# Performance work log

Hardware: AMD Instinct MI355X
Metric: run time of the kernel (lower is better)

Reference implementation:

```python
import jax, jax.numpy as jnp
import numpy as np

NEG_SLOPE = 0.01  # torch F.leaky_relu default


def _mlp_block(x, mask, W, b):
    # x: [B,P,V,F]; mask: [B,P,V] bool; W: [H,F]; b: [H]
    h = jax.nn.leaky_relu(jnp.einsum('bpvf,hf->bpvh', x, W) + b, NEG_SLOPE)
    m = mask[..., None]
    out = jnp.where(m, h, 0.0)                                   # zeros at masked-out slots
    neg = jnp.where(m, out, -jnp.inf)
    pool = jnp.max(neg, axis=2, keepdims=True)                   # [B,P,1,H] masked max-pool
    any_valid = jnp.any(mask, axis=2)[:, :, None, None]
    pool = jnp.where(any_valid, pool, 0.0)                       # fully-masked polylines -> 0
    rep = jnp.broadcast_to(pool, out.shape)
    return jnp.concatenate([out, rep], axis=-1)                  # [B,P,V,2H]


def setup_inputs() -> dict:
    key = jax.random.key(0)
    ks = jax.random.split(key, 8)
    B, P, V, F, H = 32, 512, 32, 16, 64
    input_var = jax.random.normal(ks[0], (B, P, V, F), dtype=jnp.float32)
    input_mask = jax.random.bernoulli(ks[1], 0.8, (B, P, V))
    s = 1.0 / np.sqrt(F)
    W1 = jax.random.uniform(ks[2], (H, F), jnp.float32, -s, s)
    b1 = jax.random.uniform(ks[3], (H,), jnp.float32, -s, s)
    s2 = 1.0 / np.sqrt(2 * H)
    W2 = jax.random.uniform(ks[4], (H, 2 * H), jnp.float32, -s2, s2)
    b2 = jax.random.uniform(ks[5], (H,), jnp.float32, -s2, s2)
    W3 = jax.random.uniform(ks[6], (H, 2 * H), jnp.float32, -s2, s2)
    b3 = jax.random.uniform(ks[7], (H,), jnp.float32, -s2, s2)
    return {"input_var": input_var, "input_mask": input_mask,
            "W1": W1, "b1": b1, "W2": W2, "b2": b2, "W3": W3, "b3": b3,
            "size1": P, "size2": V}


def reference(input_var, input_mask, W1, b1, W2, b2, W3, b3, size1, size2):
    hidden = W1.shape[0]
    x = _mlp_block(input_var, input_mask, W1, b1)
    y = _mlp_block(x, input_mask, W2, b2)
    z = _mlp_block(y, input_mask, W3, b3)
    out = z[:, :, 0, -hidden:]                                   # pooled half, same across V
    out = jnp.where(jnp.any(input_mask, axis=2)[..., None], out, 0.0)
    return out
```

## Files before the change

### kernel.cpp

```cpp
#include <hip/hip_runtime.h>
#include <math.h>

namespace {

typedef _Float16 f16x8 __attribute__((ext_vector_type(8)));
typedef _Float16 f16x2 __attribute__((ext_vector_type(2)));
typedef float    f32x16 __attribute__((ext_vector_type(16)));
typedef unsigned int uint;

__device__ __forceinline__ uint pkrtz(float a, float b) {
    return __builtin_bit_cast(uint, __builtin_amdgcn_cvt_pkrtz(a, b));
}
__device__ __forceinline__ uint pk_add(uint a, uint b) {
    uint r; asm("v_pk_add_f16 %0, %1, %2" : "=v"(r) : "v"(a), "v"(b)); return r;
}
__device__ __forceinline__ uint pk_mul(uint a, uint b) {
    uint r; asm("v_pk_mul_f16 %0, %1, %2" : "=v"(r) : "v"(a), "v"(b)); return r;
}
__device__ __forceinline__ uint pk_max(uint a, uint b) {
    uint r; asm("v_pk_max_f16 %0, %1, %2" : "=v"(r) : "v"(a), "v"(b)); return r;
}

__global__ void prep_pack(const float* __restrict__ W1, const float* __restrict__ W2,
                          const float* __restrict__ W3, const int* __restrict__ M,
                          unsigned short* __restrict__ wsW, uint* __restrict__ wsM)
{
    int t = blockIdx.x * blockDim.x + threadIdx.x;
    if (t < 34 * 64) {
        int f = t >> 6, l = t & 63, nb = l & 31, kg = l >> 5;
        const float* src; int K, ki, nt2;
        if (f < 2)       { src = W1; K = 16;  ki = 0;           nt2 = f; }
        else if (f < 18) { int g = f - 2;  src = W2; K = 128; ki = g >> 1; nt2 = g & 1; }
        else             { int g = f - 18; src = W3; K = 128; ki = g >> 1; nt2 = g & 1; }
        const float* s = src + (size_t)(32 * nt2 + nb) * K + 16 * ki + 8 * kg;
        uint4 q;
        q.x = pkrtz(s[0], s[1]); q.y = pkrtz(s[2], s[3]);
        q.z = pkrtz(s[4], s[5]); q.w = pkrtz(s[6], s[7]);
        *(uint4*)(wsW + (size_t)f * 512 + l * 8) = q;
    } else if (t < 34 * 64 + 16384) {
        int bp = t - 34 * 64;
        const int4* mp = (const int4*)(M + bp * 32);
        uint bits = 0;
        #pragma unroll
        for (int i = 0; i < 8; ++i) {
            int4 v = mp[i];
            bits |= ((v.x ? 1u : 0u) | (v.y ? 2u : 0u) |
                     (v.z ? 4u : 0u) | (v.w ? 8u : 0u)) << (4 * i);
        }
        wsM[bp] = bits;
    }
}

__global__ __launch_bounds__(256, 3) void fused_mlp_v10(
    const float* __restrict__ X, const uint* __restrict__ MPK,
    const unsigned short* __restrict__ WF,
    const float* __restrict__ B1, const float* __restrict__ B2,
    const float* __restrict__ B3, float* __restrict__ OUT)
{
    __shared__ __align__(16) unsigned char sXb[4][2][4096];
    __shared__ __align__(16) _Float16 sP[4][2][64];

    const int t = threadIdx.x, w = t >> 6, l = t & 63;
    const int hb = l >> 5, mtl = (l >> 4) & 1;
    const size_t bp0 = (size_t)blockIdx.x * 8 + w * 2;

    unsigned char* sb[2] = { &sXb[w][0][0], &sXb[w][1][0] };
    _Float16*     pl[2] = { &sP[w][0][0],  &sP[w][1][0]  };

    uint wb0 = (uint)((l & 7) * 32 + mtl * 256 + ((l >> 3) & 1) * 1024 + hb * 8);
    wb0 ^= (uint)(mtl << 5);
    const uint wb1 = (wb0 + 512u) ^ 64u;
    const uint rb = (uint)(mtl * 2048 + hb * 1024 + ((l & 15) >> 1) * 4);
    const uint sel = (l & 1) ? 0x07060302u : 0x05040100u;
    const uint SL2 = pkrtz(0.01f, 0.01f);

    bool anyv[2]; uint adm[2][4][2];
    #pragma unroll
    for (int u = 0; u < 2; ++u) {
        uint mk = MPK[bp0 + u];
        anyv[u] = (mk != 0u);
        #pragma unroll
        for (int g = 0; g < 4; ++g) {
            uint nib = (mk >> (8 * g + 4 * hb)) & 15u;
            adm[u][g][0] = (nib & 1u ? 0u : 0xFC00u) | (nib & 2u ? 0u : 0xFC000000u);
            adm[u][g][1] = (nib & 4u ? 0u : 0xFC00u) | (nib & 8u ? 0u : 0xFC000000u);
        }
    }

    f16x8 a1f[2];
    #pragma unroll
    for (int u = 0; u < 2; ++u) {
        const float4* xp = (const float4*)(X + ((bp0 + u) * 32 + (l & 31)) * 16 + 8 * hb);
        float4 x0 = xp[0], x1 = xp[1];
        uint4 q;
        q.x = pkrtz(x0.x, x0.y); q.y = pkrtz(x0.z, x0.w);
        q.z = pkrtz(x1.x, x1.y); q.w = pkrtz(x1.z, x1.w);
        a1f[u] = __builtin_bit_cast(f16x8, q);
    }

    f32x16 zc;
    #pragma unroll
    for (int i = 0; i < 16; ++i) zc[i] = 0.f;

    f32x16 acc[2][2];

    {
        const _Float16* wp = (const _Float16*)WF + l * 8;
        f16x8 wf0 = *(const f16x8*)wp;
        f16x8 wf1 = *(const f16x8*)(wp + 512);
        #pragma unroll
        for (int u = 0; u < 2; ++u) {
            acc[u][0] = __builtin_amdgcn_mfma_f32_32x32x16_f16(a1f[u], wf0, zc, 0, 0, 0);
            acc[u][1] = __builtin_amdgcn_mfma_f32_32x32x16_f16(a1f[u], wf1, zc, 0, 0, 0);
        }
    }

    auto epi = [&](int u, const float* __restrict__ Bp, bool dostore) {
        unsigned char* sbu = sb[u];
        _Float16* plu = pl[u];
        #pragma unroll
        for (int nt2 = 0; nt2 < 2; ++nt2) {
            float bsc = Bp[32 * nt2 + (l & 31)];
            uint bpk = pkrtz(bsc, bsc);
            uint base = nt2 ? wb1 : wb0;
            uint pp = 0xFC00FC00u;
            #pragma unroll
            for (int g = 0; g < 4; ++g) {
                uint d01 = pkrtz(acc[u][nt2][4 * g + 0], acc[u][nt2][4 * g + 1]);
                uint d23 = pkrtz(acc[u][nt2][4 * g + 2], acc[u][nt2][4 * g + 3]);
                d01 = pk_add(d01, bpk);  d23 = pk_add(d23, bpk);
                d01 = pk_max(d01, pk_mul(d01, SL2));
                d23 = pk_max(d23, pk_mul(d23, SL2));
                if (dostore) {
                    uint2 st; st.x = d01; st.y = d23;
                    *(uint2*)(sbu + base + (g >> 1) * 2048 + (g & 1) * 16) = st;
                }
                pp = pk_max(pp, pk_add(d01, adm[u][g][0]));
                pp = pk_max(pp, pk_add(d23, adm[u][g][1]));
            }
            f16x2 ph = __builtin_bit_cast(f16x2, pp);
            float pv = fmaxf((float)ph[0], (float)ph[1]);
            pv = fmaxf(pv, __shfl_xor(pv, 32));
            pv = anyv[u] ? pv : 0.f;
            if (dostore) {
                if (l < 32) plu[32 * nt2 + (l & 31)] = (_Float16)pv;
            } else {
                if (l < 32) OUT[(bp0 + u) * 64 + 32 * nt2 + (l & 31)] = pv;
            }
        }
    };

    auto layerK = [&](int fb) {
        #pragma unroll
        for (int ki = 0; ki < 8; ++ki) {
            const _Float16* wp = (const _Float16*)WF + (size_t)(fb + 2 * ki) * 512 + l * 8;
            f16x8 wf0 = *(const f16x8*)wp;
            f16x8 wf1 = *(const f16x8*)(wp + 512);
            #pragma unroll
            for (int u = 0; u < 2; ++u) {
                f16x8 a;
                if (ki < 4) {
                    const unsigned char* p = sb[u] + rb + 256 * ki;
                    uint F0 = *(const uint*)(p + 32 * (0 ^ ki));
                    uint F1 = *(const uint*)(p + 32 * (1 ^ ki));
                    uint F2 = *(const uint*)(p + 32 * (2 ^ ki));
                    uint F3 = *(const uint*)(p + 32 * (3 ^ ki));
                    uint F4 = *(const uint*)(p + 32 * (4 ^ ki));
                    uint F5 = *(const uint*)(p + 32 * (5 ^ ki));
                    uint F6 = *(const uint*)(p + 32 * (6 ^ ki));
                    uint F7 = *(const uint*)(p + 32 * (7 ^ ki));
                    uint4 q;
                    q.x = __builtin_amdgcn_perm(F1, F0, sel);
                    q.y = __builtin_amdgcn_perm(F3, F2, sel);
                    q.z = __builtin_amdgcn_perm(F5, F4, sel);
                    q.w = __builtin_amdgcn_perm(F7, F6, sel);
                    a = __builtin_bit_cast(f16x8, q);
                } else {
                    a = *(const f16x8*)(pl[u] + 16 * (ki - 4) + 8 * hb);
                }
                acc[u][0] = __builtin_amdgcn_mfma_f32_32x32x16_f16(
                    a, wf0, ki == 0 ? zc : acc[u][0], 0, 0, 0);
                acc[u][1] = __builtin_amdgcn_mfma_f32_32x32x16_f16(
                    a, wf1, ki == 0 ? zc : acc[u][1], 0, 0, 0);
            }
        }
    };

    epi(0, B1, true);  epi(1, B1, true);
    layerK(2);
    epi(0, B2, true);  epi(1, B2, true);
    layerK(18);
    epi(0, B3, false); epi(1, B3, false);
}
}

extern "C" void kernel_launch(void* const* d_in, const int* in_sizes, int n_in,
                              void* d_out, int out_size, void* d_ws, size_t ws_size,
                              hipStream_t stream) {
    (void)in_sizes; (void)n_in; (void)ws_size; (void)out_size;
    const float* X  = (const float*)d_in[0];
    const int*   M  = (const int*)d_in[1];
    const float* W1 = (const float*)d_in[2];
    const float* B1 = (const float*)d_in[3];
    const float* W2 = (const float*)d_in[4];
    const float* B2 = (const float*)d_in[5];
    const float* W3 = (const float*)d_in[6];
    const float* B3 = (const float*)d_in[7];
    float* OUT = (float*)d_out;

    unsigned short* WF  = (unsigned short*)d_ws;
    uint*           MPK = (uint*)((char*)d_ws + 34816);

    prep_pack<<<(34 * 64 + 16384 + 255) / 256, 256, 0, stream>>>(W1, W2, W3, M, WF, MPK);
    fused_mlp_v10<<<2048, 256, 0, stream>>>(X, MPK, WF, B1, B2, B3, OUT);
}
```

Baseline: 114.8 us.

## Preload layer weights into registers and re-swizzle LDS to avoid bank conflicts

Layer-2 weight fragments (16 uint4 per lane) now load into registers at kernel start. Layer-3 weights are refilled into those registers while layer 2 runs its MFMAs, so weight fetches no longer sit on the critical path. The LDS store and read addresses get an extra XOR swizzle to cut bank conflicts during the transpose-style reads. The launch bound drops from 3 to 2 waves per SIMD to leave room for the larger register footprint, which lowers occupancy.

```diff
diff --git a/kernel.cpp b/kernel.cpp
--- a/kernel.cpp
+++ b/kernel.cpp
@@ -51,7 +51,7 @@
     }
 }
 
-__global__ __launch_bounds__(256, 3) void fused_mlp_v10(
+__global__ __launch_bounds__(256, 2) void fused_mlp_v16(
     const float* __restrict__ X, const uint* __restrict__ MPK,
     const unsigned short* __restrict__ WF,
     const float* __restrict__ B1, const float* __restrict__ B2,
@@ -61,18 +61,27 @@
     __shared__ __align__(16) _Float16 sP[4][2][64];
 
     const int t = threadIdx.x, w = t >> 6, l = t & 63;
-    const int hb = l >> 5, mtl = (l >> 4) & 1;
+    const int hb = l >> 5, mtl = (l >> 4) & 1, l3 = (l >> 3) & 1;
     const size_t bp0 = (size_t)blockIdx.x * 8 + w * 2;
 
     unsigned char* sb[2] = { &sXb[w][0][0], &sXb[w][1][0] };
     _Float16*     pl[2] = { &sP[w][0][0],  &sP[w][1][0]  };
 
-    uint wb0 = (uint)((l & 7) * 32 + mtl * 256 + ((l >> 3) & 1) * 1024 + hb * 8);
-    wb0 ^= (uint)(mtl << 5);
+    uint wb0 = (uint)((l & 7) * 32 + mtl * 256 + l3 * 1024 + hb * 8);
+    wb0 ^= (uint)((mtl << 5) ^ (l3 << 4));
     const uint wb1 = (wb0 + 512u) ^ 64u;
-    const uint rb = (uint)(mtl * 2048 + hb * 1024 + ((l & 15) >> 1) * 4);
+    uint rbA = (uint)(mtl * 2048 + hb * 1024 + ((l & 15) >> 1) * 4);
+    rbA ^= (uint)((hb << 4) ^ (mtl << 5));
+    const uint rbB = rbA ^ 32u;
     const uint sel = (l & 1) ? 0x07060302u : 0x05040100u;
     const uint SL2 = pkrtz(0.01f, 0.01f);
+
+    const unsigned short* WFb = WF + l * 8;
+
+    uint4 wreg[16];
+    #pragma unroll
+    for (int f = 0; f < 16; ++f)
+        wreg[f] = *(const uint4*)(WFb + (size_t)(2 + f) * 512);
 
     bool anyv[2]; uint adm[2][4][2];
     #pragma unroll
@@ -105,9 +114,8 @@
     f32x16 acc[2][2];
 
     {
-        const _Float16* wp = (const _Float16*)WF + l * 8;
-        f16x8 wf0 = *(const f16x8*)wp;
-        f16x8 wf1 = *(const f16x8*)(wp + 512);
+        f16x8 wf0 = *(const f16x8*)(WFb);
+        f16x8 wf1 = *(const f16x8*)(WFb + 512);
         #pragma unroll
         for (int u = 0; u < 2; ++u) {
             acc[u][0] = __builtin_amdgcn_mfma_f32_32x32x16_f16(a1f[u], wf0, zc, 0, 0, 0);
@@ -132,8 +140,10 @@
                 d01 = pk_max(d01, pk_mul(d01, SL2));
                 d23 = pk_max(d23, pk_mul(d23, SL2));
                 if (dostore) {
+                    uint wba = (base ^ (uint)(((g & 1) << 4) ^ ((g >> 1) << 5)))
+                               + (uint)((g >> 1) * 2048);
                     uint2 st; st.x = d01; st.y = d23;
-                    *(uint2*)(sbu + base + (g >> 1) * 2048 + (g & 1) * 16) = st;
+                    *(uint2*)(sbu + wba) = st;
                 }
                 pp = pk_max(pp, pk_add(d01, adm[u][g][0]));
                 pp = pk_max(pp, pk_add(d23, adm[u][g][1]));
@@ -150,30 +160,28 @@
         }
     };
 
-    auto layerK = [&](int fb) {
+    auto layerK = [&](bool refill, int fb_next) {
         #pragma unroll
         for (int ki = 0; ki < 8; ++ki) {
-            const _Float16* wp = (const _Float16*)WF + (size_t)(fb + 2 * ki) * 512 + l * 8;
-            f16x8 wf0 = *(const f16x8*)wp;
-            f16x8 wf1 = *(const f16x8*)(wp + 512);
+            f16x8 wf0 = __builtin_bit_cast(f16x8, wreg[2 * ki]);
+            f16x8 wf1 = __builtin_bit_cast(f16x8, wreg[2 * ki + 1]);
             #pragma unroll
             for (int u = 0; u < 2; ++u) {
                 f16x8 a;
                 if (ki < 4) {
-                    const unsigned char* p = sb[u] + rb + 256 * ki;
-                    uint F0 = *(const uint*)(p + 32 * (0 ^ ki));
-                    uint F1 = *(const uint*)(p + 32 * (1 ^ ki));
-                    uint F2 = *(const uint*)(p + 32 * (2 ^ ki));
-                    uint F3 = *(const uint*)(p + 32 * (3 ^ ki));
-                    uint F4 = *(const uint*)(p + 32 * (4 ^ ki));
-                    uint F5 = *(const uint*)(p + 32 * (5 ^ ki));
-                    uint F6 = *(const uint*)(p + 32 * (6 ^ ki));
-                    uint F7 = *(const uint*)(p + 32 * (7 ^ ki));
+                    const unsigned char* pA = sb[u] + rbA + 256 * ki;
+                    const unsigned char* pB = sb[u] + rbB + 256 * ki;
+                    uint F[8];
+                    #pragma unroll
+                    for (int j = 0; j < 8; ++j) {
+                        const int e = j ^ ki;
+                        F[j] = *(const uint*)(((e & 1) ? pB : pA) + 32 * (e & ~1));
+                    }
                     uint4 q;
-                    q.x = __builtin_amdgcn_perm(F1, F0, sel);
-                    q.y = __builtin_amdgcn_perm(F3, F2, sel);
-                    q.z = __builtin_amdgcn_perm(F5, F4, sel);
-                    q.w = __builtin_amdgcn_perm(F7, F6, sel);
+                    q.x = __builtin_amdgcn_perm(F[1], F[0], sel);
+                    q.y = __builtin_amdgcn_perm(F[3], F[2], sel);
+                    q.z = __builtin_amdgcn_perm(F[5], F[4], sel);
+                    q.w = __builtin_amdgcn_perm(F[7], F[6], sel);
                     a = __builtin_bit_cast(f16x8, q);
                 } else {
                     a = *(const f16x8*)(pl[u] + 16 * (ki - 4) + 8 * hb);
@@ -183,13 +191,17 @@
                 acc[u][1] = __builtin_amdgcn_mfma_f32_32x32x16_f16(
                     a, wf1, ki == 0 ? zc : acc[u][1], 0, 0, 0);
             }
+            if (refill) {
+                wreg[2 * ki]     = *(const uint4*)(WFb + (size_t)(fb_next + 2 * ki) * 512);
+                wreg[2 * ki + 1] = *(const uint4*)(WFb + (size_t)(fb_next + 2 * ki + 1) * 512);
+            }
         }
     };
 
     epi(0, B1, true);  epi(1, B1, true);
-    layerK(2);
+    layerK(true, 18);
     epi(0, B2, true);  epi(1, B2, true);
-    layerK(18);
+    layerK(false, 0);
     epi(0, B3, false); epi(1, B3, false);
 }
 }
@@ -212,5 +224,5 @@
     uint*           MPK = (uint*)((char*)d_ws + 34816);
 
     prep_pack<<<(34 * 64 + 16384 + 255) / 256, 256, 0, stream>>>(W1, W2, W3, M, WF, MPK);
-    fused_mlp_v10<<<2048, 256, 0, stream>>>(X, MPK, WF, B1, B2, B3, OUT);
-}
+    fused_mlp_v16<<<2048, 256, 0, stream>>>(X, MPK, WF, B1, B2, B3, OUT);
+}
```

Result: no change. 114.3 us (-0.4%).
